# Kernel optimization log

Hardware: AMD Instinct MI355X
Metric: run time of the kernel (lower is better)

Reference implementation:

```python
import jax, jax.numpy as jnp
import numpy as np

IN_DIM = 96
HIDDEN = 256
EPS = 1e-6
NEG = -1e10


def setup_inputs() -> dict:
    key = jax.random.key(0)
    ks = jax.random.split(key, 12)
    B, S = 8, 2048
    q = jax.random.normal(ks[0], (B, S, IN_DIM), dtype=jnp.float32)
    k = jax.random.normal(ks[1], (B, S, IN_DIM), dtype=jnp.float32)
    v = jax.random.normal(ks[2], (B, S, IN_DIM), dtype=jnp.float32)
    mask = jax.random.randint(ks[3], (B, S, S), 0, 2, dtype=jnp.int32)
    s = 1.0 / np.sqrt(IN_DIM)
    Wq = jax.random.normal(ks[4], (IN_DIM, HIDDEN), dtype=jnp.float32) * s
    bq = jax.random.normal(ks[5], (HIDDEN,), dtype=jnp.float32) * 0.01
    Wk = jax.random.normal(ks[6], (IN_DIM, HIDDEN), dtype=jnp.float32) * s
    bk = jax.random.normal(ks[7], (HIDDEN,), dtype=jnp.float32) * 0.01
    Wv = jax.random.normal(ks[8], (IN_DIM, HIDDEN), dtype=jnp.float32) * s
    bv = jax.random.normal(ks[9], (HIDDEN,), dtype=jnp.float32) * 0.01
    gamma = jnp.ones((HIDDEN,), dtype=jnp.float32)
    beta = jnp.zeros((HIDDEN,), dtype=jnp.float32)
    return {"query": q, "key": k, "value": v, "mask": mask,
            "Wq": Wq, "bq": bq, "Wk": Wk, "bk": bk, "Wv": Wv, "bv": bv,
            "gamma": gamma, "beta": beta}


def reference(query, key, value, mask, Wq, bq, Wk, bk, Wv, bv, gamma, beta):
    # Linear projections: [B,S,96] @ [96,H] -> [B,S,H]
    q = jnp.einsum('bsf,fh->bsh', query, Wq) + bq
    k = jnp.einsum('bsf,fh->bsh', key, Wk) + bk
    v = jnp.einsum('bsf,fh->bsh', value, Wv) + bv
    # Scaled dot-product scores: [B,S,S]
    score = jnp.einsum('bqh,bkh->bqk', q, k) / jnp.sqrt(jnp.float32(HIDDEN))
    score = jnp.where(mask == 0, jnp.float32(NEG), score)
    attn = jax.nn.softmax(score, axis=-1)
    out = jnp.einsum('bqk,bkh->bqh', attn, v)
    # LayerNorm over last dim, eps=1e-6
    mu = jnp.mean(out, axis=-1, keepdims=True)
    var = jnp.mean(jnp.square(out - mu), axis=-1, keepdims=True)
    normed = (out - mu) * jax.lax.rsqrt(var + EPS)
    return normed * gamma + beta
```

## Files before the change

kernel.cpp:

```cpp
#include <hip/hip_runtime.h>

#define B_   8
#define S_   2048
#define IN_  96
#define H_   256
#define NROW (B_ * S_)

typedef float    f32x4 __attribute__((ext_vector_type(4)));
typedef _Float16 f16x8 __attribute__((ext_vector_type(8)));

__device__ __forceinline__ unsigned short f2h(float x) {
    return __builtin_bit_cast(unsigned short, (_Float16)x);
}
__device__ __forceinline__ float h2f(unsigned short x) {
    return (float)__builtin_bit_cast(_Float16, x);
}
__device__ __forceinline__ void lds_barrier() {
    asm volatile("s_waitcnt lgkmcnt(0)\n\ts_barrier" ::: "memory");
}
__device__ __forceinline__ int4 nt_load_int4(const int* p) {
    long long v0 = __builtin_nontemporal_load((const long long*)p);
    long long v1 = __builtin_nontemporal_load(((const long long*)p) + 1);
    int4 r;
    r.x = (int)(v0 & 0xffffffffLL); r.y = (int)(v0 >> 32);
    r.z = (int)(v1 & 0xffffffffLL); r.w = (int)(v1 >> 32);
    return r;
}

__global__ __launch_bounds__(256) void wconv_kernel(
    const float* __restrict__ Wq, const float* __restrict__ Wk,
    const float* __restrict__ Wv, unsigned short* __restrict__ wt)
{
    const int p  = blockIdx.x >> 3;
    const int h0 = (blockIdx.x & 7) * 32;
    const float* W = (p == 0) ? Wq : (p == 1) ? Wk : Wv;
    unsigned short* dst = wt + (size_t)p * H_ * IN_ + (size_t)h0 * IN_;

    __shared__ unsigned short lds[32][100];
    const int t = threadIdx.x;
    #pragma unroll
    for (int i = 0; i < 12; ++i) {
        int idx = i * 256 + t;
        int f = idx >> 5;
        int hl = idx & 31;
        lds[hl][f] = f2h(W[f * H_ + h0 + hl]);
    }
    __syncthreads();
    #pragma unroll
    for (int j = 0; j < 6; ++j) {
        int e = (j * 256 + t) * 2;
        int hl = e / IN_, f = e % IN_;
        unsigned int pk = (unsigned int)lds[hl][f] |
                          ((unsigned int)lds[hl][f + 1] << 16);
        ((unsigned int*)dst)[j * 256 + t] = pk;
    }
}

__global__ __launch_bounds__(256) void proj_kernel3(
    const float* __restrict__ query, const float* __restrict__ key,
    const float* __restrict__ value, const unsigned short* __restrict__ wt,
    const float* __restrict__ bq, const float* __restrict__ bk,
    const float* __restrict__ bv,
    unsigned short* __restrict__ pq, unsigned short* __restrict__ pk,
    unsigned short* __restrict__ pv)
{
    __shared__ unsigned short Xs[3][16][104];

    const int t    = threadIdx.x;
    const int lane = t & 63;
    const int wave = t >> 6;
    const int col  = lane & 15;
    const int quad = lane >> 4;
    const int bi   = blockIdx.x;
    const int s0   = bi * 16;
    const int b    = s0 >> 11;
    const int sl   = s0 & (S_ - 1);

    const float* srcs[3] = { query + (size_t)s0 * IN_,
                             key   + (size_t)s0 * IN_,
                             value + (size_t)s0 * IN_ };
    #pragma unroll
    for (int p = 0; p < 3; ++p) {
        #pragma unroll
        for (int i = 0; i < 2; ++i) {
            int idx = i * 256 + t;
            if (idx < 384) {
                f32x4 x = *(const f32x4*)(srcs[p] + idx * 4);
                int r = idx / 24;
                int f = (idx - r * 24) * 4;
                unsigned long long pkk =
                    (unsigned long long)f2h(x[0])
                  | ((unsigned long long)f2h(x[1]) << 16)
                  | ((unsigned long long)f2h(x[2]) << 32)
                  | ((unsigned long long)f2h(x[3]) << 48);
                *(unsigned long long*)&Xs[p][r][f] = pkk;
            }
        }
    }
    __syncthreads();

    const int hc = wave;
    #pragma unroll
    for (int p = 0; p < 3; ++p) {
        const unsigned short* wbase = wt + (size_t)p * H_ * IN_;
        f16x8 wfr[4][3];
        #pragma unroll
        for (int ht = 0; ht < 4; ++ht)
            #pragma unroll
            for (int kc = 0; kc < 3; ++kc)
                wfr[ht][kc] = *(const f16x8*)(wbase
                    + (size_t)(hc * 64 + ht * 16 + col) * IN_ + kc * 32 + quad * 8);
        f16x8 xfr[3];
        #pragma unroll
        for (int kc = 0; kc < 3; ++kc)
            xfr[kc] = *(const f16x8*)&Xs[p][col][kc * 32 + quad * 8];

        f32x4 acc[4];
        #pragma unroll
        for (int ht = 0; ht < 4; ++ht) acc[ht] = (f32x4)(0.0f);
        #pragma unroll
        for (int kc = 0; kc < 3; ++kc)
            #pragma unroll
            for (int ht = 0; ht < 4; ++ht)
                acc[ht] = (p < 2)
                    ? __builtin_amdgcn_mfma_f32_16x16x32_f16(xfr[kc], wfr[ht][kc], acc[ht], 0, 0, 0)
                    : __builtin_amdgcn_mfma_f32_16x16x32_f16(wfr[ht][kc], xfr[kc], acc[ht], 0, 0, 0);

        if (p < 2) {
            unsigned short* dst  = (p == 0) ? pq : pk;
            const float*    bias = (p == 0) ? bq : bk;
            #pragma unroll
            for (int ht = 0; ht < 4; ++ht) {
                float bh = bias[hc * 64 + ht * 16 + col];
                const int s    = hc * 2 + (ht >> 1);
                const int lq   = ((ht & 1) * 2 + (col >> 3)) * 16;
                const int j    = col & 7;
                #pragma unroll
                for (int r = 0; r < 4; ++r)
                    dst[(size_t)(((bi * 8 + s) * 64 + lq + quad * 4 + r)) * 8 + j]
                        = f2h(acc[ht][r] + bh);
            }
        } else {
            const int kl  = (sl & 63) + col;
            const int c   = sl >> 6;
            const int s2  = kl >> 5;
            const int qv  = (kl >> 3) & 3;
            const int jj  = col & 7;
            #pragma unroll
            for (int ht = 0; ht < 4; ++ht) {
                f32x4 b4 = *(const f32x4*)(bv + hc * 64 + ht * 16 + quad * 4);
                #pragma unroll
                for (int r = 0; r < 4; ++r)
                    pv[(size_t)(((b * 32 + c) * 32 + hc * 8 + ht * 2 + s2) * 64
                                + qv * 16 + quad * 4 + r) * 8 + jj]
                        = f2h(acc[ht][r] + b4[r]);
            }
        }
    }
}

__global__ __launch_bounds__(256, 2) void attn_kernel(
    const unsigned short* __restrict__ pq, const unsigned short* __restrict__ pk,
    const unsigned short* __restrict__ pv, const int* __restrict__ mask,
    unsigned short* __restrict__ Opart, float* __restrict__ lpart)
{
    __shared__ unsigned short P[2][32][68];
    __shared__ float lsum[4][32];

    const int tid  = threadIdx.x;
    const int wave = tid >> 6;
    const int lane = tid & 63;
    const int col  = lane & 15;
    const int quad = lane >> 4;

    const int b     = blockIdx.x & 7;
    const int strip = (blockIdx.x >> 3) & 63;
    const int kh    = blockIdx.x >> 9;
    const int q0    = strip << 5;

    f16x8 qf[2][8];
    #pragma unroll
    for (int st = 0; st < 2; ++st) {
        const unsigned short* qb = pq + (size_t)(b * 128 + strip * 2 + st) * 4096
                                      + lane * 8;
        #pragma unroll
        for (int s = 0; s < 8; ++s) qf[st][s] = *(const f16x8*)(qb + s * 512);
    }

    f32x4 O[2][4];
    #pragma unroll
    for (int st = 0; st < 2; ++st)
        #pragma unroll
        for (int ht = 0; ht < 4; ++ht) O[st][ht] = (f32x4)(0.0f);
    float l0 = 0.0f, l1 = 0.0f;

    const unsigned short* pkb = pk + (size_t)(b * 128) * 4096 + lane * 8;
    const unsigned short* pvb = pv + (size_t)(b * 32) * 32 * 512
                                   + (size_t)wave * 8 * 512 + lane * 8;
    const int* mb0 = mask + (size_t)(b * S_ + q0 + col) * S_ + kh * 1024
                   + wave * 16 + quad * 4;
    const int* mb1 = mb0 + 16 * S_;

    f16x8 kf[2][8];
    #pragma unroll
    for (int s = 0; s < 8; ++s)
        kf[0][s] = *(const f16x8*)(pkb + (size_t)(kh * 64 + wave) * 4096 + s * 512);

    int4 mc0 = nt_load_int4(mb0);
    int4 mc1 = nt_load_int4(mb1);

    #pragma unroll 2
    for (int c = 0; c < 16; ++c) {
        const int pb = c & 1;
        const int cn = (c < 15) ? c + 1 : c;
        const int gc = kh * 16 + c;

        {
            const unsigned short* kb = pkb + (size_t)(kh * 64 + cn * 4 + wave) * 4096;
            #pragma unroll
            for (int s = 0; s < 8; ++s)
                kf[pb ^ 1][s] = *(const f16x8*)(kb + s * 512);
        }

        const unsigned short* vb = pvb + (size_t)gc * 32 * 512;
        f16x8 vf[4][2];
        #pragma unroll
        for (int ht = 0; ht < 4; ++ht)
            #pragma unroll
            for (int s2 = 0; s2 < 2; ++s2)
                vf[ht][s2] = *(const f16x8*)(vb + (size_t)(ht * 2 + s2) * 512);

        int4 mn0 = nt_load_int4(mb0 + cn * 64);
        int4 mn1 = nt_load_int4(mb1 + cn * 64);

        f32x4 St0 = (f32x4)(0.0f), St1 = (f32x4)(0.0f);
        #pragma unroll
        for (int s = 0; s < 8; ++s) {
            St0 = __builtin_amdgcn_mfma_f32_16x16x32_f16(kf[pb][s], qf[0][s], St0, 0, 0, 0);
            St1 = __builtin_amdgcn_mfma_f32_16x16x32_f16(kf[pb][s], qf[1][s], St1, 0, 0, 0);
        }

        {
            int mi[4] = { mc0.x, mc0.y, mc0.z, mc0.w };
            unsigned long long pk64 = 0;
            #pragma unroll
            for (int r = 0; r < 4; ++r) {
                float p = (mi[r] == 0) ? 0.0f : __expf(St0[r] * 0.0625f - 6.0f);
                _Float16 ph = (_Float16)p;
                l0 += (float)ph;
                pk64 |= (unsigned long long)__builtin_bit_cast(unsigned short, ph)
                        << (16 * r);
            }
            *(unsigned long long*)&P[pb][col][wave * 16 + quad * 4] = pk64;
        }
        {
            int mi[4] = { mc1.x, mc1.y, mc1.z, mc1.w };
            unsigned long long pk64 = 0;
            #pragma unroll
            for (int r = 0; r < 4; ++r) {
                float p = (mi[r] == 0) ? 0.0f : __expf(St1[r] * 0.0625f - 6.0f);
                _Float16 ph = (_Float16)p;
                l1 += (float)ph;
                pk64 |= (unsigned long long)__builtin_bit_cast(unsigned short, ph)
                        << (16 * r);
            }
            *(unsigned long long*)&P[pb][16 + col][wave * 16 + quad * 4] = pk64;
        }
        mc0 = mn0; mc1 = mn1;

        lds_barrier();

        #pragma unroll
        for (int st = 0; st < 2; ++st) {
            #pragma unroll
            for (int s2 = 0; s2 < 2; ++s2) {
                union { unsigned long long u[2]; f16x8 v; } pu;
                const unsigned short* pr = &P[pb][st * 16 + col][s2 * 32 + quad * 8];
                pu.u[0] = *(const unsigned long long*)pr;
                pu.u[1] = *(const unsigned long long*)(pr + 4);
                f16x8 pf = pu.v;
                #pragma unroll
                for (int ht = 0; ht < 4; ++ht)
                    O[st][ht] = __builtin_amdgcn_mfma_f32_16x16x32_f16(pf, vf[ht][s2], O[st][ht], 0, 0, 0);
            }
        }
    }

    l0 += __shfl_xor(l0, 16); l0 += __shfl_xor(l0, 32);
    l1 += __shfl_xor(l1, 16); l1 += __shfl_xor(l1, 32);
    if (lane < 16) { lsum[wave][lane] = l0; lsum[wave][16 + lane] = l1; }
    __syncthreads();

    if (wave == 0 && lane < 16) {
        #pragma unroll
        for (int st = 0; st < 2; ++st) {
            float lt = lsum[0][st * 16 + lane] + lsum[1][st * 16 + lane]
                     + lsum[2][st * 16 + lane] + lsum[3][st * 16 + lane];
            lpart[(size_t)kh * NROW + b * S_ + q0 + st * 16 + lane] = lt;
        }
    }

    unsigned short* ob = Opart + (size_t)kh * NROW * H_ + (size_t)(b * S_) * H_;
    #pragma unroll
    for (int st = 0; st < 2; ++st)
        #pragma unroll
        for (int ht = 0; ht < 4; ++ht)
            #pragma unroll
            for (int r = 0; r < 4; ++r)
                ob[(size_t)(q0 + st * 16 + quad * 4 + r) * H_
                   + wave * 64 + ht * 16 + col] = f2h(O[st][ht][r]);
}

__global__ __launch_bounds__(256) void merge_ln_kernel(
    const unsigned short* __restrict__ Opart, const float* __restrict__ lpart,
    const float* __restrict__ gamma, const float* __restrict__ beta,
    float* __restrict__ out)
{
    const int R0 = blockIdx.x * 16;
    const int q  = threadIdx.x >> 4;
    const int i  = threadIdx.x & 15;

    const size_t row = (size_t)(R0 + q);
    float linv = 1.0f / (lpart[row] + lpart[NROW + row]);

    const unsigned short* o0 = Opart + row * H_;
    const unsigned short* o1 = o0 + (size_t)NROW * H_;

    float vals[16];
    float sum = 0.0f;
    #pragma unroll
    for (int j = 0; j < 16; ++j) {
        int h = j * 16 + i;
        vals[j] = (h2f(o0[h]) + h2f(o1[h])) * linv;
        sum += vals[j];
    }
    sum += __shfl_xor(sum, 1);
    sum += __shfl_xor(sum, 2);
    sum += __shfl_xor(sum, 4);
    sum += __shfl_xor(sum, 8);
    float mu = sum * (1.0f / H_);
    float sq = 0.0f;
    #pragma unroll
    for (int j = 0; j < 16; ++j) {
        float d = vals[j] - mu;
        sq += d * d;
    }
    sq += __shfl_xor(sq, 1);
    sq += __shfl_xor(sq, 2);
    sq += __shfl_xor(sq, 4);
    sq += __shfl_xor(sq, 8);
    float rstd = rsqrtf(sq * (1.0f / H_) + 1e-6f);

    float* orow = out + row * H_;
    #pragma unroll
    for (int j = 0; j < 16; ++j) {
        int h = j * 16 + i;
        orow[h] = (vals[j] - mu) * rstd * gamma[h] + beta[h];
    }
}

extern "C" void kernel_launch(void* const* d_in, const int* in_sizes, int n_in,
                              void* d_out, int out_size, void* d_ws, size_t ws_size,
                              hipStream_t stream)
{
    const float* query = (const float*)d_in[0];
    const float* key   = (const float*)d_in[1];
    const float* value = (const float*)d_in[2];
    const int*   mask  = (const int*)d_in[3];
    const float* Wq = (const float*)d_in[4];
    const float* bq = (const float*)d_in[5];
    const float* Wk = (const float*)d_in[6];
    const float* bk = (const float*)d_in[7];
    const float* Wv = (const float*)d_in[8];
    const float* bv = (const float*)d_in[9];
    const float* gamma = (const float*)d_in[10];
    const float* beta  = (const float*)d_in[11];
    float* out = (float*)d_out;

    const size_t NQK = (size_t)B_ * S_ * H_;
    unsigned short* pq = (unsigned short*)d_ws;
    unsigned short* pk = pq + NQK;
    unsigned short* pv = pk + NQK;
    unsigned short* wt = pv + NQK;
    unsigned short* Op = wt + (size_t)3 * H_ * IN_;
    float*          lp = (float*)(Op + (size_t)2 * NROW * H_);

    wconv_kernel<<<24, 256, 0, stream>>>(Wq, Wk, Wv, wt);
    proj_kernel3<<<B_ * S_ / 16, 256, 0, stream>>>(query, key, value, wt,
                                                   bq, bk, bv, pq, pk, pv);
    attn_kernel<<<B_ * S_ / 32 * 2, 256, 0, stream>>>(pq, pk, pv, mask, Op, lp);
    merge_ln_kernel<<<NROW / 16, 256, 0, stream>>>(Op, lp, gamma, beta, out);
}
```

Before: 301.1 us.

## Pack mask into bitmask in projection kernel, stage Q in LDS, vectorize LN

The projection launch gains interleaved blocks that compress the int32 mask into 64-bit ballot bitmasks, so the attention kernel reads 1 bit per element instead of 4 bytes. The attention kernel moves Q fragments into LDS to free registers and raises occupancy to 3 waves per SIMD. It also drops K double buffering, uses exp2 with a folded scale, and adds setprio around the MFMA sections. The merge/LayerNorm kernel becomes one wave per row with vectorized loads and stores. The mask still has to be read in full once, now inside the projection launch, and the LDS Q reads add latency to the score loop.

```diff
diff --git a/kernel.cpp b/kernel.cpp
--- a/kernel.cpp
+++ b/kernel.cpp
@@ -17,14 +17,6 @@
 }
 __device__ __forceinline__ void lds_barrier() {
     asm volatile("s_waitcnt lgkmcnt(0)\n\ts_barrier" ::: "memory");
-}
-__device__ __forceinline__ int4 nt_load_int4(const int* p) {
-    long long v0 = __builtin_nontemporal_load((const long long*)p);
-    long long v1 = __builtin_nontemporal_load(((const long long*)p) + 1);
-    int4 r;
-    r.x = (int)(v0 & 0xffffffffLL); r.y = (int)(v0 >> 32);
-    r.z = (int)(v1 & 0xffffffffLL); r.w = (int)(v1 >> 32);
-    return r;
 }
 
 __global__ __launch_bounds__(256) void wconv_kernel(
@@ -60,10 +52,31 @@
     const float* __restrict__ query, const float* __restrict__ key,
     const float* __restrict__ value, const unsigned short* __restrict__ wt,
     const float* __restrict__ bq, const float* __restrict__ bk,
-    const float* __restrict__ bv,
+    const float* __restrict__ bv, const int* __restrict__ mask,
     unsigned short* __restrict__ pq, unsigned short* __restrict__ pk,
-    unsigned short* __restrict__ pv)
+    unsigned short* __restrict__ pv, unsigned long long* __restrict__ pm)
 {
+    const int bid = blockIdx.x;
+    if ((bid % 3) == 2) {
+        const int pb   = bid / 3;
+        const int wv   = threadIdx.x >> 6;
+        const int lane = threadIdx.x & 63;
+        const int r0   = pb * 32 + wv * 8;
+        #pragma unroll
+        for (int rr = 0; rr < 8; ++rr) {
+            const int* mrow = mask + (size_t)(r0 + rr) * S_;
+            unsigned long long* prow = pm + (size_t)(r0 + rr) * 32;
+            #pragma unroll 4
+            for (int it = 0; it < 32; ++it) {
+                int mi = __builtin_nontemporal_load(mrow + it * 64 + lane);
+                unsigned long long bb = __ballot(mi != 0);
+                if (lane == 0) prow[it] = bb;
+            }
+        }
+        return;
+    }
+    const int bi = (bid / 3) * 2 + (bid % 3);
+
     __shared__ unsigned short Xs[3][16][104];
 
     const int t    = threadIdx.x;
@@ -71,7 +84,6 @@
     const int wave = t >> 6;
     const int col  = lane & 15;
     const int quad = lane >> 4;
-    const int bi   = blockIdx.x;
     const int s0   = bi * 16;
     const int b    = s0 >> 11;
     const int sl   = s0 & (S_ - 1);
@@ -159,11 +171,12 @@
     }
 }
 
-__global__ __launch_bounds__(256, 2) void attn_kernel(
+__global__ __launch_bounds__(256, 3) void attn_kernel(
     const unsigned short* __restrict__ pq, const unsigned short* __restrict__ pk,
-    const unsigned short* __restrict__ pv, const int* __restrict__ mask,
+    const unsigned short* __restrict__ pv, const unsigned long long* __restrict__ pm,
     unsigned short* __restrict__ Opart, float* __restrict__ lpart)
 {
+    __shared__ __align__(16) unsigned short Qs[2][4096];
     __shared__ unsigned short P[2][32][68];
     __shared__ float lsum[4][32];
 
@@ -178,13 +191,13 @@
     const int kh    = blockIdx.x >> 9;
     const int q0    = strip << 5;
 
-    f16x8 qf[2][8];
-    #pragma unroll
-    for (int st = 0; st < 2; ++st) {
-        const unsigned short* qb = pq + (size_t)(b * 128 + strip * 2 + st) * 4096
-                                      + lane * 8;
-        #pragma unroll
-        for (int s = 0; s < 8; ++s) qf[st][s] = *(const f16x8*)(qb + s * 512);
+    {
+        const unsigned short* qsrc = pq + (size_t)(b * 128 + strip * 2) * 4096;
+        #pragma unroll
+        for (int ph = 0; ph < 4; ++ph) {
+            int i = ph * 2048 + tid * 8;
+            *(f16x8*)&((unsigned short*)Qs)[i] = *(const f16x8*)(qsrc + i);
+        }
     }
 
     f32x4 O[2][4];
@@ -197,17 +210,22 @@
     const unsigned short* pkb = pk + (size_t)(b * 128) * 4096 + lane * 8;
     const unsigned short* pvb = pv + (size_t)(b * 32) * 32 * 512
                                    + (size_t)wave * 8 * 512 + lane * 8;
-    const int* mb0 = mask + (size_t)(b * S_ + q0 + col) * S_ + kh * 1024
-                   + wave * 16 + quad * 4;
-    const int* mb1 = mb0 + 16 * S_;
-
-    f16x8 kf[2][8];
+
+    const unsigned* pm32 = (const unsigned*)pm;
+    const int sh = (wave & 1) * 16 + quad * 4;
+    const unsigned* mp0 = pm32 + (size_t)(b * S_ + q0 + col) * 64
+                        + kh * 32 + (wave >> 1);
+    const unsigned* mp1 = mp0 + 16 * 64;
+
+    f16x8 kf[8];
     #pragma unroll
     for (int s = 0; s < 8; ++s)
-        kf[0][s] = *(const f16x8*)(pkb + (size_t)(kh * 64 + wave) * 4096 + s * 512);
-
-    int4 mc0 = nt_load_int4(mb0);
-    int4 mc1 = nt_load_int4(mb1);
+        kf[s] = *(const f16x8*)(pkb + (size_t)(kh * 64 + wave) * 4096 + s * 512);
+
+    unsigned mw0 = mp0[0];
+    unsigned mw1 = mp1[0];
+
+    __syncthreads();
 
     #pragma unroll 2
     for (int c = 0; c < 16; ++c) {
@@ -215,37 +233,42 @@
         const int cn = (c < 15) ? c + 1 : c;
         const int gc = kh * 16 + c;
 
+        const unsigned short* vb = pvb + (size_t)gc * 32 * 512;
+        f16x8 vf[4][2];
+        #pragma unroll
+        for (int ht = 0; ht < 4; ++ht)
+            #pragma unroll
+            for (int s2 = 0; s2 < 2; ++s2)
+                vf[ht][s2] = *(const f16x8*)(vb + (size_t)(ht * 2 + s2) * 512);
+
+        unsigned mn0 = mp0[cn * 2];
+        unsigned mn1 = mp1[cn * 2];
+
+        f32x4 St0 = (f32x4)(0.0f), St1 = (f32x4)(0.0f);
+        __builtin_amdgcn_s_setprio(1);
+        #pragma unroll
+        for (int s = 0; s < 8; ++s) {
+            f16x8 q0f = *(const f16x8*)&Qs[0][s * 512 + lane * 8];
+            f16x8 q1f = *(const f16x8*)&Qs[1][s * 512 + lane * 8];
+            St0 = __builtin_amdgcn_mfma_f32_16x16x32_f16(kf[s], q0f, St0, 0, 0, 0);
+            St1 = __builtin_amdgcn_mfma_f32_16x16x32_f16(kf[s], q1f, St1, 0, 0, 0);
+        }
+        __builtin_amdgcn_s_setprio(0);
+
         {
             const unsigned short* kb = pkb + (size_t)(kh * 64 + cn * 4 + wave) * 4096;
             #pragma unroll
             for (int s = 0; s < 8; ++s)
-                kf[pb ^ 1][s] = *(const f16x8*)(kb + s * 512);
-        }
-
-        const unsigned short* vb = pvb + (size_t)gc * 32 * 512;
-        f16x8 vf[4][2];
-        #pragma unroll
-        for (int ht = 0; ht < 4; ++ht)
-            #pragma unroll
-            for (int s2 = 0; s2 < 2; ++s2)
-                vf[ht][s2] = *(const f16x8*)(vb + (size_t)(ht * 2 + s2) * 512);
-
-        int4 mn0 = nt_load_int4(mb0 + cn * 64);
-        int4 mn1 = nt_load_int4(mb1 + cn * 64);
-
-        f32x4 St0 = (f32x4)(0.0f), St1 = (f32x4)(0.0f);
-        #pragma unroll
-        for (int s = 0; s < 8; ++s) {
-            St0 = __builtin_amdgcn_mfma_f32_16x16x32_f16(kf[pb][s], qf[0][s], St0, 0, 0, 0);
-            St1 = __builtin_amdgcn_mfma_f32_16x16x32_f16(kf[pb][s], qf[1][s], St1, 0, 0, 0);
+                kf[s] = *(const f16x8*)(kb + s * 512);
         }
 
         {
-            int mi[4] = { mc0.x, mc0.y, mc0.z, mc0.w };
+            unsigned bits = mw0 >> sh;
             unsigned long long pk64 = 0;
             #pragma unroll
             for (int r = 0; r < 4; ++r) {
-                float p = (mi[r] == 0) ? 0.0f : __expf(St0[r] * 0.0625f - 6.0f);
+                float e = exp2f(fmaf(St0[r], 0.0901679843f, -8.65617025f));
+                float p = ((bits >> r) & 1u) ? e : 0.0f;
                 _Float16 ph = (_Float16)p;
                 l0 += (float)ph;
                 pk64 |= (unsigned long long)__builtin_bit_cast(unsigned short, ph)
@@ -254,11 +277,12 @@
             *(unsigned long long*)&P[pb][col][wave * 16 + quad * 4] = pk64;
         }
         {
-            int mi[4] = { mc1.x, mc1.y, mc1.z, mc1.w };
+            unsigned bits = mw1 >> sh;
             unsigned long long pk64 = 0;
             #pragma unroll
             for (int r = 0; r < 4; ++r) {
-                float p = (mi[r] == 0) ? 0.0f : __expf(St1[r] * 0.0625f - 6.0f);
+                float e = exp2f(fmaf(St1[r], 0.0901679843f, -8.65617025f));
+                float p = ((bits >> r) & 1u) ? e : 0.0f;
                 _Float16 ph = (_Float16)p;
                 l1 += (float)ph;
                 pk64 |= (unsigned long long)__builtin_bit_cast(unsigned short, ph)
@@ -266,10 +290,11 @@
             }
             *(unsigned long long*)&P[pb][16 + col][wave * 16 + quad * 4] = pk64;
         }
-        mc0 = mn0; mc1 = mn1;
+        mw0 = mn0; mw1 = mn1;
 
         lds_barrier();
 
+        __builtin_amdgcn_s_setprio(1);
         #pragma unroll
         for (int st = 0; st < 2; ++st) {
             #pragma unroll
@@ -284,6 +309,7 @@
                     O[st][ht] = __builtin_amdgcn_mfma_f32_16x16x32_f16(pf, vf[ht][s2], O[st][ht], 0, 0, 0);
             }
         }
+        __builtin_amdgcn_s_setprio(0);
     }
 
     l0 += __shfl_xor(l0, 16); l0 += __shfl_xor(l0, 32);
@@ -316,47 +342,47 @@
     const float* __restrict__ gamma, const float* __restrict__ beta,
     float* __restrict__ out)
 {
-    const int R0 = blockIdx.x * 16;
-    const int q  = threadIdx.x >> 4;
-    const int i  = threadIdx.x & 15;
-
-    const size_t row = (size_t)(R0 + q);
+    const int row  = blockIdx.x * 4 + (threadIdx.x >> 6);
+    const int lane = threadIdx.x & 63;
+
     float linv = 1.0f / (lpart[row] + lpart[NROW + row]);
 
-    const unsigned short* o0 = Opart + row * H_;
+    const unsigned short* o0 = Opart + (size_t)row * H_ + lane * 4;
     const unsigned short* o1 = o0 + (size_t)NROW * H_;
-
-    float vals[16];
+    unsigned long long a0 = *(const unsigned long long*)o0;
+    unsigned long long a1 = *(const unsigned long long*)o1;
+
+    float vals[4];
     float sum = 0.0f;
     #pragma unroll
-    for (int j = 0; j < 16; ++j) {
-        int h = j * 16 + i;
-        vals[j] = (h2f(o0[h]) + h2f(o1[h])) * linv;
+    for (int j = 0; j < 4; ++j) {
+        vals[j] = (h2f((unsigned short)(a0 >> (16 * j)))
+                 + h2f((unsigned short)(a1 >> (16 * j)))) * linv;
         sum += vals[j];
     }
-    sum += __shfl_xor(sum, 1);
-    sum += __shfl_xor(sum, 2);
-    sum += __shfl_xor(sum, 4);
-    sum += __shfl_xor(sum, 8);
+    sum += __shfl_xor(sum, 1);  sum += __shfl_xor(sum, 2);
+    sum += __shfl_xor(sum, 4);  sum += __shfl_xor(sum, 8);
+    sum += __shfl_xor(sum, 16); sum += __shfl_xor(sum, 32);
     float mu = sum * (1.0f / H_);
+
     float sq = 0.0f;
     #pragma unroll
-    for (int j = 0; j < 16; ++j) {
+    for (int j = 0; j < 4; ++j) {
         float d = vals[j] - mu;
         sq += d * d;
     }
-    sq += __shfl_xor(sq, 1);
-    sq += __shfl_xor(sq, 2);
-    sq += __shfl_xor(sq, 4);
-    sq += __shfl_xor(sq, 8);
+    sq += __shfl_xor(sq, 1);  sq += __shfl_xor(sq, 2);
+    sq += __shfl_xor(sq, 4);  sq += __shfl_xor(sq, 8);
+    sq += __shfl_xor(sq, 16); sq += __shfl_xor(sq, 32);
     float rstd = rsqrtf(sq * (1.0f / H_) + 1e-6f);
 
-    float* orow = out + row * H_;
-    #pragma unroll
-    for (int j = 0; j < 16; ++j) {
-        int h = j * 16 + i;
-        orow[h] = (vals[j] - mu) * rstd * gamma[h] + beta[h];
-    }
+    f32x4 g  = *(const f32x4*)(gamma + lane * 4);
+    f32x4 be = *(const f32x4*)(beta  + lane * 4);
+    f32x4 o;
+    #pragma unroll
+    for (int j = 0; j < 4; ++j)
+        o[j] = (vals[j] - mu) * rstd * g[j] + be[j];
+    *(f32x4*)(out + (size_t)row * H_ + lane * 4) = o;
 }
 
 extern "C" void kernel_launch(void* const* d_in, const int* in_sizes, int n_in,
@@ -384,10 +410,11 @@
     unsigned short* wt = pv + NQK;
     unsigned short* Op = wt + (size_t)3 * H_ * IN_;
     float*          lp = (float*)(Op + (size_t)2 * NROW * H_);
+    unsigned long long* pm = (unsigned long long*)(lp + 2 * NROW);
 
     wconv_kernel<<<24, 256, 0, stream>>>(Wq, Wk, Wv, wt);
-    proj_kernel3<<<B_ * S_ / 16, 256, 0, stream>>>(query, key, value, wt,
-                                                   bq, bk, bv, pq, pk, pv);
-    attn_kernel<<<B_ * S_ / 32 * 2, 256, 0, stream>>>(pq, pk, pv, mask, Op, lp);
-    merge_ln_kernel<<<NROW / 16, 256, 0, stream>>>(Op, lp, gamma, beta, out);
-}
+    proj_kernel3<<<1536, 256, 0, stream>>>(query, key, value, wt,
+                                           bq, bk, bv, mask, pq, pk, pv, pm);
+    attn_kernel<<<B_ * S_ / 32 * 2, 256, 0, stream>>>(pq, pk, pv, pm, Op, lp);
+    merge_ln_kernel<<<NROW / 4, 256, 0, stream>>>(Op, lp, gamma, beta, out);
+}
```

After: 416.2 us. 38.2% more time.
